# Kernel tuning notes

Hardware: AMD Instinct MI355X
Metric: run time of the kernel (lower is better)

Reference implementation:

```python
import math
import jax, jax.numpy as jnp
import numpy as np

NUM_HEADS = 16
LN_EPS = 1e-5


def _ln(x, g, b):
    m = x.mean(-1, keepdims=True)
    v = ((x - m) ** 2).mean(-1, keepdims=True)
    return (x - m) * jax.lax.rsqrt(v + LN_EPS) * g + b


def _rotary_embedding(lat, lon, dim, base=10000.0):
    # spherical-geometry-aware rotary phases; returns sin/cos of shape lat.shape + [dim//2]
    pi = jnp.asarray(math.pi, lat.dtype)
    lon_wrapped = jnp.remainder(lon + pi, 2 * pi) - pi
    lat_c = jnp.clip(lat, -math.pi / 2 + 1e-6, math.pi / 2 - 1e-6)
    scaled_lon = lon_wrapped * jnp.cos(lat_c)
    half = dim // 2
    inv_freq = 1.0 / (base ** (jnp.arange(half, dtype=lat.dtype) / half))
    phase = (lat_c + scaled_lon)[..., None] * inv_freq
    return jnp.sin(phase), jnp.cos(phase)


def _apply_rotary(q, k, sin, cos):
    # q,k: [N, heads, S, hd]; sin/cos: [S, hd//2]
    sin = sin[None, None]
    cos = cos[None, None]
    def rot(x):
        x1 = x[..., 0::2]  # even lanes (torch view(...,hd//2,2).unbind(-1))
        x2 = x[..., 1::2]
        # torch concatenates the two rotated halves (no re-interleave)
        return jnp.concatenate([x1 * cos - x2 * sin, x1 * sin + x2 * cos], axis=-1)
    return rot(q), rot(k)


def _sdpa(q, k, v):
    scale = 1.0 / jnp.sqrt(jnp.asarray(q.shape[-1], q.dtype))
    s = jnp.einsum('nhqd,nhkd->nhqk', q, k) * scale
    return jnp.einsum('nhqk,nhkd->nhqd', jax.nn.softmax(s, axis=-1), v)


def _axial_block(tokens, g, bln, qkv_w, qkv_b, proj_w, proj_b, sincos):
    # tokens: [N, S, D] -> norm -> qkv -> (rope) -> sdpa -> proj -> residual
    N, S, D = tokens.shape
    hd = D // NUM_HEADS
    qkv = _ln(tokens, g, bln) @ qkv_w + qkv_b
    q, k, v = jnp.split(qkv, 3, axis=-1)
    def to_heads(t):
        return t.reshape(N, S, NUM_HEADS, hd).transpose(0, 2, 1, 3)
    q, k, v = to_heads(q), to_heads(k), to_heads(v)
    if sincos is not None:
        q, k = _apply_rotary(q, k, sincos[0], sincos[1])
    o = _sdpa(q, k, v).transpose(0, 2, 1, 3).reshape(N, S, D)
    return tokens + (o @ proj_w + proj_b)


def setup_inputs() -> dict:
    key = jax.random.key(0)
    ks = jax.random.split(key, 8)
    B, L, H, W, D = 1, 13, 48, 96, 512
    x = jax.random.normal(ks[0], (B, L, H, W, D), dtype=jnp.float32)
    lat_grid = jnp.linspace(-math.pi / 2 + 0.01, math.pi / 2 - 0.01, H, dtype=jnp.float32)
    lon_grid = jnp.linspace(-math.pi, math.pi, W, dtype=jnp.float32)  # unused by forward
    s = 0.02
    return {
        'x': x, 'lat_grid': lat_grid, 'lon_grid': lon_grid,
        'lat_qkv_w': s * jax.random.normal(ks[1], (D, 3 * D), jnp.float32),
        'lat_qkv_b': jnp.zeros((3 * D,), jnp.float32),
        'lon_qkv_w': s * jax.random.normal(ks[2], (D, 3 * D), jnp.float32),
        'lon_qkv_b': jnp.zeros((3 * D,), jnp.float32),
        'lev_qkv_w': s * jax.random.normal(ks[3], (D, 3 * D), jnp.float32),
        'lev_qkv_b': jnp.zeros((3 * D,), jnp.float32),
        'proj_w': s * jax.random.normal(ks[4], (D, D), jnp.float32),
        'proj_b': jnp.zeros((D,), jnp.float32),
        'g_lat': jnp.ones((D,), jnp.float32), 'b_lat': jnp.zeros((D,), jnp.float32),
        'g_lon': jnp.ones((D,), jnp.float32), 'b_lon': jnp.zeros((D,), jnp.float32),
        'g_lev': jnp.ones((D,), jnp.float32), 'b_lev': jnp.zeros((D,), jnp.float32),
    }


def reference(x, lat_grid, lon_grid, lat_qkv_w, lat_qkv_b, lon_qkv_w, lon_qkv_b,
              lev_qkv_w, lev_qkv_b, proj_w, proj_b,
              g_lat, b_lat, g_lon, b_lon, g_lev, b_lev):
    B, L, H, W, D = x.shape
    hd = D // NUM_HEADS
    # --- lat axis ---
    lat_tokens = x.transpose(0, 1, 3, 2, 4).reshape(B * L * W, H, D)
    lat_sin, lat_cos = _rotary_embedding(lat_grid, jnp.zeros_like(lat_grid), hd)
    lat_out = _axial_block(lat_tokens, g_lat, b_lat, lat_qkv_w, lat_qkv_b,
                           proj_w, proj_b, (lat_sin, lat_cos))
    lat_out = lat_out.reshape(B, L, W, H, D).transpose(0, 1, 3, 2, 4)
    # --- lon axis ---
    lon_tokens = lat_out.reshape(B * L * H, W, D)
    lon_range = jnp.linspace(-math.pi, math.pi, W, dtype=x.dtype)
    lon_sin, lon_cos = _rotary_embedding(jnp.zeros_like(lon_range), lon_range, hd)
    lon_out = _axial_block(lon_tokens, g_lon, b_lon, lon_qkv_w, lon_qkv_b,
                           proj_w, proj_b, (lon_sin, lon_cos))
    lon_out = lon_out.reshape(B, L, H, W, D)
    # --- level axis (no rotary) ---
    lev_tokens = lon_out.transpose(0, 2, 3, 1, 4).reshape(B * H * W, L, D)
    lev_out = _axial_block(lev_tokens, g_lev, b_lev, lev_qkv_w, lev_qkv_b,
                           proj_w, proj_b, None)
    return lev_out.reshape(B, H, W, L, D).transpose(0, 3, 1, 2, 4)
```

## Files before the change

### kernel.cpp

```cpp
#include <hip/hip_runtime.h>
#include <cstdint>


#define L_DIM 13
#define H_DIM 48
#define W_DIM 96
#define D_DIM 512
#define NH    16
#define MTOK  (L_DIM * H_DIM * W_DIM)
#define N3    (3 * D_DIM)
#define PI_F  3.14159265358979323846f

typedef __bf16 bf16x8 __attribute__((ext_vector_type(8)));
typedef float  f32x4  __attribute__((ext_vector_type(4)));

__device__ __forceinline__ float bf2f(unsigned short u) {
    return __builtin_bit_cast(float, ((unsigned)u) << 16);
}
__device__ __forceinline__ unsigned short f2bf(float f) {
    unsigned u = __builtin_bit_cast(unsigned, f);
    u += 0x7fffu + ((u >> 16) & 1u);
    return (unsigned short)(u >> 16);
}
__device__ __forceinline__ void gload16(unsigned short* lds, const unsigned short* g) {
    __builtin_amdgcn_global_load_lds(
        (const __attribute__((address_space(1))) unsigned int*)g,
        (__attribute__((address_space(3))) unsigned int*)lds, 16, 0, 0);
}

__global__ __launch_bounds__(256) void transpose_w(const float* __restrict__ w,
                                                   unsigned short* __restrict__ wt, int N) {
    __shared__ unsigned short t[64][65];
    const int k0 = blockIdx.x * 64, n0 = blockIdx.y * 64;
    const int tid = threadIdx.x;
    #pragma unroll
    for (int j = 0; j < 16; ++j) {
        int lin = j * 256 + tid;
        int kr = lin >> 6, nc = lin & 63;
        t[kr][nc] = f2bf(w[(size_t)(k0 + kr) * N + n0 + nc]);
    }
    __syncthreads();
    #pragma unroll
    for (int j = 0; j < 16; ++j) {
        int lin = j * 256 + tid;
        int nr = lin >> 6, kc = lin & 63;
        wt[(size_t)(n0 + nr) * 512 + k0 + kc] = t[kc][nr];
    }
}

__global__ __launch_bounds__(256) void ln_apply(
    const float* __restrict__ src, const float* __restrict__ g,
    const float* __restrict__ bln, unsigned short* __restrict__ out)
{
    int wv = threadIdx.x >> 6, lane = threadIdx.x & 63;
    int t = blockIdx.x * 4 + wv;
    const float* p = src + (size_t)t * 512 + lane * 8;
    float4 a = *(const float4*)p, b = *(const float4*)(p + 4);
    float s  = a.x + a.y + a.z + a.w + b.x + b.y + b.z + b.w;
    float s2 = a.x*a.x + a.y*a.y + a.z*a.z + a.w*a.w + b.x*b.x + b.y*b.y + b.z*b.z + b.w*b.w;
    #pragma unroll
    for (int off = 1; off < 64; off <<= 1) {
        s  += __shfl_xor(s, off, 64);
        s2 += __shfl_xor(s2, off, 64);
    }
    float mu = s * (1.f / 512.f);
    float rs = rsqrtf(s2 * (1.f / 512.f) - mu * mu + 1e-5f);
    float4 g0 = *(const float4*)(g + lane * 8),  g1 = *(const float4*)(g + lane * 8 + 4);
    float4 b0 = *(const float4*)(bln + lane * 8), b1 = *(const float4*)(bln + lane * 8 + 4);
    unsigned short o[8];
    o[0] = f2bf((a.x - mu) * rs * g0.x + b0.x);
    o[1] = f2bf((a.y - mu) * rs * g0.y + b0.y);
    o[2] = f2bf((a.z - mu) * rs * g0.z + b0.z);
    o[3] = f2bf((a.w - mu) * rs * g0.w + b0.w);
    o[4] = f2bf((b.x - mu) * rs * g1.x + b1.x);
    o[5] = f2bf((b.y - mu) * rs * g1.y + b1.y);
    o[6] = f2bf((b.z - mu) * rs * g1.z + b1.z);
    o[7] = f2bf((b.w - mu) * rs * g1.w + b1.w);
    uint4 r;
    r.x = (unsigned)o[0] | ((unsigned)o[1] << 16);
    r.y = (unsigned)o[2] | ((unsigned)o[3] << 16);
    r.z = (unsigned)o[4] | ((unsigned)o[5] << 16);
    r.w = (unsigned)o[6] | ((unsigned)o[7] << 16);
    *(uint4*)&out[(size_t)t * 512 + lane * 8] = r;
}

__global__ __launch_bounds__(256) void qkv_gemm(
    const unsigned short* __restrict__ lnb,
    const unsigned short* __restrict__ wT, const float* __restrict__ bias,
    unsigned short* __restrict__ out)
{
    __shared__ alignas(16) unsigned short As[128][64];
    __shared__ alignas(16) unsigned short Bs[128][64];
    const int n0 = blockIdx.x * 128, m0 = blockIdx.y * 128;
    const int tid = threadIdx.x, lane = tid & 63, wv = tid >> 6;
    const int wm = (wv >> 1) * 64, wn = (wv & 1) * 64;
    const int srow = lane >> 3;
    const int scol = (((lane & 7) ^ srow) << 3);
    f32x4 acc[4][4] = {};

    for (int k0 = 0; k0 < 512; k0 += 64) {
        #pragma unroll
        for (int i = 0; i < 4; ++i) {
            int c = i * 4 + wv;
            int r = c * 8 + srow;
            gload16(&As[c * 8][0], &lnb[(size_t)(m0 + r) * 512 + k0 + scol]);
            gload16(&Bs[c * 8][0], &wT [(size_t)(n0 + r) * 512 + k0 + scol]);
        }
        __syncthreads();
        const int ko = (lane >> 4) * 8, lm = lane & 15, sw = lm & 7;
        #pragma unroll
        for (int kk = 0; kk < 64; kk += 32) {
            const int cA = ((((kk + ko) >> 3) ^ sw) << 3);
            bf16x8 af[4], bfr[4];
            #pragma unroll
            for (int mi = 0; mi < 4; ++mi) af[mi]  = *(const bf16x8*)&As[wm + mi * 16 + lm][cA];
            #pragma unroll
            for (int ni = 0; ni < 4; ++ni) bfr[ni] = *(const bf16x8*)&Bs[wn + ni * 16 + lm][cA];
            #pragma unroll
            for (int mi = 0; mi < 4; ++mi)
                #pragma unroll
                for (int ni = 0; ni < 4; ++ni)
                    acc[mi][ni] = __builtin_amdgcn_mfma_f32_16x16x32_bf16(af[mi], bfr[ni], acc[mi][ni], 0, 0, 0);
        }
        __syncthreads();
    }
    const int cr = (lane >> 4) * 4, ccol = lane & 15;
    #pragma unroll
    for (int ni = 0; ni < 4; ++ni) {
        int col = n0 + wn + ni * 16 + ccol;
        float bb = bias[col];
        #pragma unroll
        for (int mi = 0; mi < 4; ++mi)
            #pragma unroll
            for (int r = 0; r < 4; ++r) {
                int row = m0 + wm + mi * 16 + cr + r;
                out[(size_t)row * N3 + col] = f2bf(acc[mi][ni][r] + bb);
            }
    }
}

template<int S, int MODE>
__global__ __launch_bounds__(256) void attn_big(
    unsigned short* __restrict__ qkv,
    const float* __restrict__ lat_grid, const float* __restrict__ lon_grid)
{
    constexpr int NQ  = S / 16;
    constexpr int SKP = (S + 31) & ~31;
    constexpr int VST = SKP + 8;
    __shared__ alignas(16) unsigned short qs[S][40];
    __shared__ alignas(16) unsigned short ks[S][40];
    __shared__ alignas(16) unsigned short vT[32][VST];
    __shared__ alignas(16) unsigned short pb[4][16][VST];

    const int n = blockIdx.x, h = blockIdx.y;
    const int tid = threadIdx.x, lane = tid & 63, wv = tid >> 6;
    int base, step;
    if (MODE == 0) { int l = n / 96, w = n - l * 96; base = l * 4608 + w; step = 96; }
    else           { base = n * 96; step = 1; }

    const float SCALE = 0.17677669529663689f;
    for (int idx = tid; idx < S * 16; idx += 256) {
        int s = idx >> 4, i = idx & 15;
        size_t ro = (size_t)(base + s * step) * N3 + h * 32;
        unsigned qp = *(const unsigned*)(qkv + ro + 2 * i);
        unsigned kp = *(const unsigned*)(qkv + ro + 512 + 2 * i);
        unsigned vp = *(const unsigned*)(qkv + ro + 1024 + 2 * i);
        float coord;
        if (MODE == 0) {
            float la = lat_grid[s];
            coord = fminf(fmaxf(la, -PI_F / 2 + 1e-6f), PI_F / 2 - 1e-6f);
        } else {
            float xp = lon_grid[s] + PI_F;
            coord = xp - floorf(xp * (0.5f / PI_F)) * (2.f * PI_F) - PI_F;
        }
        float ph = coord * exp2f(-(float)i * 0.83048202372f);
        float sn = sinf(ph), cs = cosf(ph);
        float q1 = bf2f((unsigned short)qp), q2 = bf2f((unsigned short)(qp >> 16));
        float k1 = bf2f((unsigned short)kp), k2 = bf2f((unsigned short)(kp >> 16));
        qs[s][i]      = f2bf((q1 * cs - q2 * sn) * SCALE);
        qs[s][16 + i] = f2bf((q1 * sn + q2 * cs) * SCALE);
        ks[s][i]      = f2bf(k1 * cs - k2 * sn);
        ks[s][16 + i] = f2bf(k1 * sn + k2 * cs);
        vT[2 * i][s]     = (unsigned short)vp;
        vT[2 * i + 1][s] = (unsigned short)(vp >> 16);
    }
    if (SKP > S) {
        for (int idx = tid; idx < 32 * (SKP - S); idx += 256)
            vT[idx / (SKP - S)][S + idx % (SKP - S)] = 0;
    }
    __syncthreads();

    const int lm = lane & 15, ko = (lane >> 4) * 8, q4 = (lane >> 4) * 4;
    f32x4 zero = {0.f, 0.f, 0.f, 0.f};
    bf16x8 vf[SKP / 32][2];
    #pragma unroll
    for (int u2 = 0; u2 < SKP / 32; ++u2)
        #pragma unroll
        for (int nh2 = 0; nh2 < 2; ++nh2)
            vf[u2][nh2] = *(const bf16x8*)&vT[nh2 * 16 + lm][u2 * 32 + ko];
    if (SKP > S) {
        for (int idx = lane; idx < 16 * (SKP - S); idx += 64)
            pb[wv][idx / (SKP - S)][S + idx % (SKP - S)] = 0;
    }

    for (int t = wv; t < NQ; t += 4) {
        bf16x8 aq = *(const bf16x8*)&qs[t * 16 + lm][ko];
        f32x4 c[NQ];
        #pragma unroll
        for (int u = 0; u < NQ; ++u) {
            bf16x8 bk = *(const bf16x8*)&ks[u * 16 + lm][ko];
            c[u] = __builtin_amdgcn_mfma_f32_16x16x32_bf16(aq, bk, zero, 0, 0, 0);
        }
        float mr[4] = {-1e30f, -1e30f, -1e30f, -1e30f}, sm[4] = {0.f, 0.f, 0.f, 0.f};
        #pragma unroll
        for (int u = 0; u < NQ; ++u)
            #pragma unroll
            for (int r = 0; r < 4; ++r) mr[r] = fmaxf(mr[r], c[u][r]);
        #pragma unroll
        for (int r = 0; r < 4; ++r)
            #pragma unroll
            for (int off = 1; off < 16; off <<= 1)
                mr[r] = fmaxf(mr[r], __shfl_xor(mr[r], off, 64));
        #pragma unroll
        for (int u = 0; u < NQ; ++u)
            #pragma unroll
            for (int r = 0; r < 4; ++r) {
                float e = __expf(c[u][r] - mr[r]);
                c[u][r] = e; sm[r] += e;
            }
        #pragma unroll
        for (int r = 0; r < 4; ++r) {
            #pragma unroll
            for (int off = 1; off < 16; off <<= 1)
                sm[r] += __shfl_xor(sm[r], off, 64);
            sm[r] = 1.f / sm[r];
        }
        #pragma unroll
        for (int u = 0; u < NQ; ++u)
            #pragma unroll
            for (int r = 0; r < 4; ++r)
                pb[wv][q4 + r][u * 16 + lm] = f2bf(c[u][r] * sm[r]);
        __builtin_amdgcn_wave_barrier();
        f32x4 o0 = zero, o1 = zero;
        #pragma unroll
        for (int u2 = 0; u2 < SKP / 32; ++u2) {
            bf16x8 ap = *(const bf16x8*)&pb[wv][lm][u2 * 32 + ko];
            o0 = __builtin_amdgcn_mfma_f32_16x16x32_bf16(ap, vf[u2][0], o0, 0, 0, 0);
            o1 = __builtin_amdgcn_mfma_f32_16x16x32_bf16(ap, vf[u2][1], o1, 0, 0, 0);
        }
        __builtin_amdgcn_wave_barrier();
        #pragma unroll
        for (int r = 0; r < 4; ++r) {
            int row = t * 16 + q4 + r;
            size_t ro = (size_t)(base + row * step) * N3 + h * 32;
            qkv[ro + lm]      = f2bf(o0[r]);
            qkv[ro + 16 + lm] = f2bf(o1[r]);
        }
    }
}

__global__ __launch_bounds__(256) void attn_small(unsigned short* __restrict__ qkv)
{
    __shared__ alignas(16) unsigned short qs[4][16][40];
    __shared__ alignas(16) unsigned short ks[4][16][40];
    __shared__ alignas(16) unsigned short vT[4][32][40];
    __shared__ alignas(16) unsigned short pb[4][16][40];
    const int tid = threadIdx.x, lane = tid & 63, wv = tid >> 6;
    const int pair = blockIdx.x * 4 + wv;
    const int n = pair >> 4, h = pair & 15;
    const int base = n, step = 4608;

    for (int idx = lane; idx < 13 * 16; idx += 64) {
        int s = idx >> 4, i = idx & 15;
        size_t ro = (size_t)(base + s * step) * N3 + h * 32;
        *(unsigned*)&qs[wv][s][2 * i] = *(const unsigned*)(qkv + ro + 2 * i);
        *(unsigned*)&ks[wv][s][2 * i] = *(const unsigned*)(qkv + ro + 512 + 2 * i);
        unsigned vp = *(const unsigned*)(qkv + ro + 1024 + 2 * i);
        vT[wv][2 * i][s]     = (unsigned short)vp;
        vT[wv][2 * i + 1][s] = (unsigned short)(vp >> 16);
    }
    for (int idx = lane; idx < 32 * 19; idx += 64) {
        int d = idx / 19, k = 13 + idx % 19;
        vT[wv][d][k] = 0;
    }
    for (int idx = lane; idx < 16 * 16; idx += 64)
        pb[wv][idx >> 4][16 + (idx & 15)] = 0;
    __syncthreads();

    const int lm = lane & 15, ko = (lane >> 4) * 8, q4 = (lane >> 4) * 4;
    f32x4 zero = {0.f, 0.f, 0.f, 0.f};
    bf16x8 aq = *(const bf16x8*)&qs[wv][lm][ko];
    bf16x8 bk = *(const bf16x8*)&ks[wv][lm][ko];
    f32x4 c = __builtin_amdgcn_mfma_f32_16x16x32_bf16(aq, bk, zero, 0, 0, 0);
    const float SCALE = 0.17677669529663689f;
    float cf[4], mr[4], sm[4];
    bool colok = (lm < 13);
    #pragma unroll
    for (int r = 0; r < 4; ++r) {
        cf[r] = colok ? c[r] * SCALE : -1e30f;
        mr[r] = cf[r];
    }
    #pragma unroll
    for (int r = 0; r < 4; ++r)
        #pragma unroll
        for (int off = 1; off < 16; off <<= 1)
            mr[r] = fmaxf(mr[r], __shfl_xor(mr[r], off, 64));
    #pragma unroll
    for (int r = 0; r < 4; ++r) { cf[r] = __expf(cf[r] - mr[r]); sm[r] = cf[r]; }
    #pragma unroll
    for (int r = 0; r < 4; ++r) {
        #pragma unroll
        for (int off = 1; off < 16; off <<= 1)
            sm[r] += __shfl_xor(sm[r], off, 64);
        sm[r] = 1.f / sm[r];
    }
    #pragma unroll
    for (int r = 0; r < 4; ++r)
        pb[wv][q4 + r][lm] = f2bf(cf[r] * sm[r]);
    __builtin_amdgcn_wave_barrier();
    bf16x8 ap  = *(const bf16x8*)&pb[wv][lm][ko];
    bf16x8 vf0 = *(const bf16x8*)&vT[wv][lm][ko];
    bf16x8 vf1 = *(const bf16x8*)&vT[wv][16 + lm][ko];
    f32x4 o0 = __builtin_amdgcn_mfma_f32_16x16x32_bf16(ap, vf0, zero, 0, 0, 0);
    f32x4 o1 = __builtin_amdgcn_mfma_f32_16x16x32_bf16(ap, vf1, zero, 0, 0, 0);
    #pragma unroll
    for (int r = 0; r < 4; ++r) {
        int row = q4 + r;
        if (row < 13) {
            size_t ro = (size_t)(base + row * step) * N3 + h * 32;
            qkv[ro + lm]      = f2bf(o0[r]);
            qkv[ro + 16 + lm] = f2bf(o1[r]);
        }
    }
}

__global__ __launch_bounds__(256) void proj_gemm(
    const unsigned short* __restrict__ attn,
    const unsigned short* __restrict__ pT, const float* __restrict__ pb,
    const float* __restrict__ resid, float* __restrict__ tok)
{
    __shared__ alignas(16) unsigned short As[128][64];
    __shared__ alignas(16) unsigned short Bs[128][64];
    const int n0 = blockIdx.x * 128, m0 = blockIdx.y * 128;
    const int tid = threadIdx.x, lane = tid & 63, wv = tid >> 6;
    const int wm = (wv >> 1) * 64, wn = (wv & 1) * 64;
    const int srow = lane >> 3;
    const int scol = (((lane & 7) ^ srow) << 3);
    f32x4 acc[4][4] = {};

    for (int k0 = 0; k0 < 512; k0 += 64) {
        #pragma unroll
        for (int i = 0; i < 4; ++i) {
            int c = i * 4 + wv;
            int r = c * 8 + srow;
            gload16(&As[c * 8][0], &attn[(size_t)(m0 + r) * N3 + k0 + scol]);
            gload16(&Bs[c * 8][0], &pT [(size_t)(n0 + r) * 512 + k0 + scol]);
        }
        __syncthreads();
        const int ko = (lane >> 4) * 8, lm = lane & 15, sw = lm & 7;
        #pragma unroll
        for (int kk = 0; kk < 64; kk += 32) {
            const int cA = ((((kk + ko) >> 3) ^ sw) << 3);
            bf16x8 af[4], bfr[4];
            #pragma unroll
            for (int mi = 0; mi < 4; ++mi) af[mi]  = *(const bf16x8*)&As[wm + mi * 16 + lm][cA];
            #pragma unroll
            for (int ni = 0; ni < 4; ++ni) bfr[ni] = *(const bf16x8*)&Bs[wn + ni * 16 + lm][cA];
            #pragma unroll
            for (int mi = 0; mi < 4; ++mi)
                #pragma unroll
                for (int ni = 0; ni < 4; ++ni)
                    acc[mi][ni] = __builtin_amdgcn_mfma_f32_16x16x32_bf16(af[mi], bfr[ni], acc[mi][ni], 0, 0, 0);
        }
        __syncthreads();
    }
    const int cr = (lane >> 4) * 4, ccol = lane & 15;
    #pragma unroll
    for (int ni = 0; ni < 4; ++ni) {
        int col = n0 + wn + ni * 16 + ccol;
        float bb = pb[col];
        #pragma unroll
        for (int mi = 0; mi < 4; ++mi)
            #pragma unroll
            for (int r = 0; r < 4; ++r) {
                int row = m0 + wm + mi * 16 + cr + r;
                size_t a = (size_t)row * 512 + col;
                tok[a] = resid[a] + acc[mi][ni][r] + bb;
            }
    }
}

extern "C" void kernel_launch(void* const* d_in, const int* in_sizes, int n_in,
                              void* d_out, int out_size, void* d_ws, size_t ws_size,
                              hipStream_t stream) {
    const float* x        = (const float*)d_in[0];
    const float* lat_grid = (const float*)d_in[1];
    const float* lon_grid = (const float*)d_in[2];
    const float* qkv_w[3] = {(const float*)d_in[3], (const float*)d_in[5], (const float*)d_in[7]};
    const float* qkv_b[3] = {(const float*)d_in[4], (const float*)d_in[6], (const float*)d_in[8]};
    const float* proj_w   = (const float*)d_in[9];
    const float* proj_b   = (const float*)d_in[10];
    const float* g[3]     = {(const float*)d_in[11], (const float*)d_in[13], (const float*)d_in[15]};
    const float* bln[3]   = {(const float*)d_in[12], (const float*)d_in[14], (const float*)d_in[16]};
    float* tok = (float*)d_out;

    unsigned short* wT0 = (unsigned short*)d_ws;
    unsigned short* wT1 = wT0 + 1536 * 512;
    unsigned short* wT2 = wT1 + 1536 * 512;
    unsigned short* pT  = wT2 + 1536 * 512;
    unsigned short* lnb = pT + 512 * 512;
    unsigned short* qkv = lnb + (size_t)MTOK * 512;
    unsigned short* wT[3] = {wT0, wT1, wT2};

    transpose_w<<<dim3(8, 24), 256, 0, stream>>>(qkv_w[0], wT0, 1536);
    transpose_w<<<dim3(8, 24), 256, 0, stream>>>(qkv_w[1], wT1, 1536);
    transpose_w<<<dim3(8, 24), 256, 0, stream>>>(qkv_w[2], wT2, 1536);
    transpose_w<<<dim3(8, 8),  256, 0, stream>>>(proj_w, pT, 512);

    for (int b = 0; b < 3; ++b) {
        const float* src = (b == 0) ? x : tok;
        ln_apply<<<MTOK / 4, 256, 0, stream>>>(src, g[b], bln[b], lnb);
        qkv_gemm<<<dim3(N3 / 128, MTOK / 128), 256, 0, stream>>>(lnb, wT[b], qkv_b[b], qkv);
        if (b == 0)
            attn_big<48, 0><<<dim3(L_DIM * W_DIM, NH), 256, 0, stream>>>(qkv, lat_grid, lon_grid);
        else if (b == 1)
            attn_big<96, 1><<<dim3(L_DIM * H_DIM, NH), 256, 0, stream>>>(qkv, lat_grid, lon_grid);
        else
            attn_small<<<(H_DIM * W_DIM * NH) / 4, 256, 0, stream>>>(qkv);
        proj_gemm<<<dim3(512 / 128, MTOK / 128), 256, 0, stream>>>(qkv, pT, proj_b, src, tok);
    }
}
```

Before: 1.239 ms.

## Replace QKV and projection GEMMs with double-buffered 256x256 pipelined MFMA kernel

Both GEMMs are replaced by one templated kernel that uses 256x256 tiles, 8 waves, and double-buffered LDS, so global loads for the next K tile overlap MFMA work on the current one. It adds XCD-aware block swizzling, s_setprio around MFMA bursts, and vectorized epilogue stores (packed bf16 and float4 residual add). The aim is to cut the memory-stall and barrier overhead of the single-buffered 128x128 kernels. The trade-off is more LDS per block, fewer blocks in flight, and delicate manual vmcnt/barrier sequencing.

```diff
diff --git a/kernel.cpp b/kernel.cpp
--- a/kernel.cpp
+++ b/kernel.cpp
@@ -84,58 +84,146 @@
     *(uint4*)&out[(size_t)t * 512 + lane * 8] = r;
 }
 
-__global__ __launch_bounds__(256) void qkv_gemm(
-    const unsigned short* __restrict__ lnb,
-    const unsigned short* __restrict__ wT, const float* __restrict__ bias,
-    unsigned short* __restrict__ out)
+#define QUAD(mi, A) do { \
+    acc[mi][0] = __builtin_amdgcn_mfma_f32_16x16x32_bf16(b0, A, acc[mi][0], 0, 0, 0); \
+    acc[mi][1] = __builtin_amdgcn_mfma_f32_16x16x32_bf16(b1, A, acc[mi][1], 0, 0, 0); \
+    acc[mi][2] = __builtin_amdgcn_mfma_f32_16x16x32_bf16(b2, A, acc[mi][2], 0, 0, 0); \
+    acc[mi][3] = __builtin_amdgcn_mfma_f32_16x16x32_bf16(b3, A, acc[mi][3], 0, 0, 0); \
+} while (0)
+#define RDA(mi, ks) (*(const bf16x8*)&As[cur][wm + (mi) * 16 + lm][((((ks) * 4 + kq) ^ (lm & 7)) << 3)])
+#define RDB(ni, ks) (*(const bf16x8*)&Bs[cur][wn + (ni) * 16 + lm][((((ks) * 4 + kq) ^ (lm & 7)) << 3)])
+
+template<int LDA, int NBX, bool PROJ>
+__global__ __launch_bounds__(512, 2) void gemm8p(
+    const unsigned short* __restrict__ A,
+    const unsigned short* __restrict__ B,
+    const float* __restrict__ bias,
+    const float* __restrict__ resid,
+    float* __restrict__ outf,
+    unsigned short* __restrict__ outh)
 {
-    __shared__ alignas(16) unsigned short As[128][64];
-    __shared__ alignas(16) unsigned short Bs[128][64];
-    const int n0 = blockIdx.x * 128, m0 = blockIdx.y * 128;
+    __shared__ alignas(16) unsigned short As[2][256][64];
+    __shared__ alignas(16) unsigned short Bs[2][256][64];
+
+    const int nwg = NBX * 234;
+    const int orig = blockIdx.y * NBX + blockIdx.x;
+    const int qq = nwg >> 3, rr = nwg & 7;
+    const int xcd = orig & 7, idx = orig >> 3;
+    const int swz = (xcd < rr ? xcd * (qq + 1) : rr * (qq + 1) + (xcd - rr) * qq) + idx;
+    const int n0 = (swz % NBX) * 256;
+    const int m0 = (swz / NBX) * 256;
+
     const int tid = threadIdx.x, lane = tid & 63, wv = tid >> 6;
-    const int wm = (wv >> 1) * 64, wn = (wv & 1) * 64;
-    const int srow = lane >> 3;
-    const int scol = (((lane & 7) ^ srow) << 3);
-    f32x4 acc[4][4] = {};
-
-    for (int k0 = 0; k0 < 512; k0 += 64) {
-        #pragma unroll
-        for (int i = 0; i < 4; ++i) {
-            int c = i * 4 + wv;
-            int r = c * 8 + srow;
-            gload16(&As[c * 8][0], &lnb[(size_t)(m0 + r) * 512 + k0 + scol]);
-            gload16(&Bs[c * 8][0], &wT [(size_t)(n0 + r) * 512 + k0 + scol]);
-        }
-        __syncthreads();
-        const int ko = (lane >> 4) * 8, lm = lane & 15, sw = lm & 7;
-        #pragma unroll
-        for (int kk = 0; kk < 64; kk += 32) {
-            const int cA = ((((kk + ko) >> 3) ^ sw) << 3);
-            bf16x8 af[4], bfr[4];
-            #pragma unroll
-            for (int mi = 0; mi < 4; ++mi) af[mi]  = *(const bf16x8*)&As[wm + mi * 16 + lm][cA];
-            #pragma unroll
-            for (int ni = 0; ni < 4; ++ni) bfr[ni] = *(const bf16x8*)&Bs[wn + ni * 16 + lm][cA];
-            #pragma unroll
-            for (int mi = 0; mi < 4; ++mi)
-                #pragma unroll
-                for (int ni = 0; ni < 4; ++ni)
-                    acc[mi][ni] = __builtin_amdgcn_mfma_f32_16x16x32_bf16(af[mi], bfr[ni], acc[mi][ni], 0, 0, 0);
-        }
-        __syncthreads();
-    }
-    const int cr = (lane >> 4) * 4, ccol = lane & 15;
-    #pragma unroll
-    for (int ni = 0; ni < 4; ++ni) {
-        int col = n0 + wn + ni * 16 + ccol;
-        float bb = bias[col];
-        #pragma unroll
-        for (int mi = 0; mi < 4; ++mi)
-            #pragma unroll
-            for (int r = 0; r < 4; ++r) {
-                int row = m0 + wm + mi * 16 + cr + r;
-                out[(size_t)row * N3 + col] = f2bf(acc[mi][ni][r] + bb);
+    const int wm = (wv >> 2) * 128, wn = (wv & 3) * 64;
+    const int lm = lane & 15, kq = lane >> 4;
+    const int rblk = lane >> 3;
+    const int sc = (((lane & 7) ^ rblk) << 3);
+
+    const unsigned short* bsrc = B + (size_t)(n0 + wv * 32 + rblk) * 512 + sc;
+    const int ar0 = (wv & 4) ? (128 + (wv & 3) * 16) : (wv * 16);
+    const unsigned short* asrc = A + (size_t)(m0 + ar0 + rblk) * LDA + sc;
+
+    f32x4 acc[8][4] = {};
+
+    #pragma unroll
+    for (int j = 0; j < 4; ++j)
+        gload16(&Bs[0][wv * 32 + j * 8][0], bsrc + (size_t)(j * 8) * 512);
+    gload16(&As[0][ar0 + 0][0], asrc);
+    gload16(&As[0][ar0 + 8][0], asrc + (size_t)8 * LDA);
+    gload16(&As[0][ar0 + 64][0], asrc + (size_t)64 * LDA);
+    gload16(&As[0][ar0 + 72][0], asrc + (size_t)72 * LDA);
+    asm volatile("s_waitcnt vmcnt(2)" ::: "memory");
+    __builtin_amdgcn_s_barrier();
+    __builtin_amdgcn_sched_barrier(0);
+
+    for (int kt = 0; kt < 8; ++kt) {
+        const int cur = kt & 1, nxt = cur ^ 1;
+        const int kn = (kt + 1) * 64;
+        const bool st = (kt < 7);
+        bf16x8 a0, a1, a2, a3, b0, b1, b2, b3;
+
+        a0 = RDA(0, 0); a1 = RDA(1, 0); a2 = RDA(2, 0); a3 = RDA(3, 0);
+        b0 = RDB(0, 0); b1 = RDB(1, 0); b2 = RDB(2, 0); b3 = RDB(3, 0);
+        if (st) {
+            gload16(&Bs[nxt][wv * 32 +  0][0], bsrc + (size_t) 0 * 512 + kn);
+            gload16(&Bs[nxt][wv * 32 +  8][0], bsrc + (size_t) 8 * 512 + kn);
+            gload16(&Bs[nxt][wv * 32 + 16][0], bsrc + (size_t)16 * 512 + kn);
+            gload16(&Bs[nxt][wv * 32 + 24][0], bsrc + (size_t)24 * 512 + kn);
+        }
+        __builtin_amdgcn_s_barrier();
+        __builtin_amdgcn_s_setprio(1);
+        QUAD(0, a0); QUAD(1, a1); QUAD(2, a2); QUAD(3, a3);
+        __builtin_amdgcn_s_setprio(0);
+        if (st) asm volatile("s_waitcnt vmcnt(4)" ::: "memory");
+        else    asm volatile("s_waitcnt vmcnt(0)" ::: "memory");
+        __builtin_amdgcn_s_barrier();
+        __builtin_amdgcn_sched_barrier(0);
+
+        a0 = RDA(4, 0); a1 = RDA(5, 0); a2 = RDA(6, 0); a3 = RDA(7, 0);
+        if (st) {
+            gload16(&As[nxt][ar0 + 0][0], asrc + kn);
+            gload16(&As[nxt][ar0 + 8][0], asrc + (size_t)8 * LDA + kn);
+        }
+        __builtin_amdgcn_s_barrier();
+        __builtin_amdgcn_s_setprio(1);
+        QUAD(4, a0); QUAD(5, a1); QUAD(6, a2); QUAD(7, a3);
+        __builtin_amdgcn_s_setprio(0);
+        __builtin_amdgcn_s_barrier();
+
+        a0 = RDA(0, 1); a1 = RDA(1, 1); a2 = RDA(2, 1); a3 = RDA(3, 1);
+        b0 = RDB(0, 1); b1 = RDB(1, 1); b2 = RDB(2, 1); b3 = RDB(3, 1);
+        if (st) {
+            gload16(&As[nxt][ar0 + 64][0], asrc + (size_t)64 * LDA + kn);
+            gload16(&As[nxt][ar0 + 72][0], asrc + (size_t)72 * LDA + kn);
+        }
+        __builtin_amdgcn_s_barrier();
+        __builtin_amdgcn_s_setprio(1);
+        QUAD(0, a0); QUAD(1, a1); QUAD(2, a2); QUAD(3, a3);
+        __builtin_amdgcn_s_setprio(0);
+        __builtin_amdgcn_s_barrier();
+
+        a0 = RDA(4, 1); a1 = RDA(5, 1); a2 = RDA(6, 1); a3 = RDA(7, 1);
+        __builtin_amdgcn_s_barrier();
+        __builtin_amdgcn_s_setprio(1);
+        QUAD(4, a0); QUAD(5, a1); QUAD(6, a2); QUAD(7, a3);
+        __builtin_amdgcn_s_setprio(0);
+        asm volatile("s_waitcnt vmcnt(2)" ::: "memory");
+        __builtin_amdgcn_s_barrier();
+        __builtin_amdgcn_sched_barrier(0);
+    }
+
+    const int cr = kq << 2;
+    if constexpr (!PROJ) {
+        #pragma unroll
+        for (int ni = 0; ni < 4; ++ni) {
+            const int col = n0 + wn + ni * 16 + cr;
+            const float4 bb = *(const float4*)&bias[col];
+            #pragma unroll
+            for (int mi = 0; mi < 8; ++mi) {
+                const size_t off = (size_t)(m0 + wm + mi * 16 + lm) * N3 + col;
+                uint2 pk;
+                pk.x = (unsigned)f2bf(acc[mi][ni][0] + bb.x) | ((unsigned)f2bf(acc[mi][ni][1] + bb.y) << 16);
+                pk.y = (unsigned)f2bf(acc[mi][ni][2] + bb.z) | ((unsigned)f2bf(acc[mi][ni][3] + bb.w) << 16);
+                *(uint2*)&outh[off] = pk;
             }
+        }
+    } else {
+        #pragma unroll
+        for (int ni = 0; ni < 4; ++ni) {
+            const int col = n0 + wn + ni * 16 + cr;
+            const float4 bb = *(const float4*)&bias[col];
+            #pragma unroll
+            for (int mi = 0; mi < 8; ++mi) {
+                const size_t off = (size_t)(m0 + wm + mi * 16 + lm) * 512 + col;
+                float4 rs = *(const float4*)&resid[off];
+                float4 o;
+                o.x = rs.x + acc[mi][ni][0] + bb.x;
+                o.y = rs.y + acc[mi][ni][1] + bb.y;
+                o.z = rs.z + acc[mi][ni][2] + bb.z;
+                o.w = rs.w + acc[mi][ni][3] + bb.w;
+                *(float4*)&outf[off] = o;
+            }
+        }
     }
 }
 
@@ -334,62 +422,6 @@
     }
 }
 
-__global__ __launch_bounds__(256) void proj_gemm(
-    const unsigned short* __restrict__ attn,
-    const unsigned short* __restrict__ pT, const float* __restrict__ pb,
-    const float* __restrict__ resid, float* __restrict__ tok)
-{
-    __shared__ alignas(16) unsigned short As[128][64];
-    __shared__ alignas(16) unsigned short Bs[128][64];
-    const int n0 = blockIdx.x * 128, m0 = blockIdx.y * 128;
-    const int tid = threadIdx.x, lane = tid & 63, wv = tid >> 6;
-    const int wm = (wv >> 1) * 64, wn = (wv & 1) * 64;
-    const int srow = lane >> 3;
-    const int scol = (((lane & 7) ^ srow) << 3);
-    f32x4 acc[4][4] = {};
-
-    for (int k0 = 0; k0 < 512; k0 += 64) {
-        #pragma unroll
-        for (int i = 0; i < 4; ++i) {
-            int c = i * 4 + wv;
-            int r = c * 8 + srow;
-            gload16(&As[c * 8][0], &attn[(size_t)(m0 + r) * N3 + k0 + scol]);
-            gload16(&Bs[c * 8][0], &pT [(size_t)(n0 + r) * 512 + k0 + scol]);
-        }
-        __syncthreads();
-        const int ko = (lane >> 4) * 8, lm = lane & 15, sw = lm & 7;
-        #pragma unroll
-        for (int kk = 0; kk < 64; kk += 32) {
-            const int cA = ((((kk + ko) >> 3) ^ sw) << 3);
-            bf16x8 af[4], bfr[4];
-            #pragma unroll
-            for (int mi = 0; mi < 4; ++mi) af[mi]  = *(const bf16x8*)&As[wm + mi * 16 + lm][cA];
-            #pragma unroll
-            for (int ni = 0; ni < 4; ++ni) bfr[ni] = *(const bf16x8*)&Bs[wn + ni * 16 + lm][cA];
-            #pragma unroll
-            for (int mi = 0; mi < 4; ++mi)
-                #pragma unroll
-                for (int ni = 0; ni < 4; ++ni)
-                    acc[mi][ni] = __builtin_amdgcn_mfma_f32_16x16x32_bf16(af[mi], bfr[ni], acc[mi][ni], 0, 0, 0);
-        }
-        __syncthreads();
-    }
-    const int cr = (lane >> 4) * 4, ccol = lane & 15;
-    #pragma unroll
-    for (int ni = 0; ni < 4; ++ni) {
-        int col = n0 + wn + ni * 16 + ccol;
-        float bb = pb[col];
-        #pragma unroll
-        for (int mi = 0; mi < 4; ++mi)
-            #pragma unroll
-            for (int r = 0; r < 4; ++r) {
-                int row = m0 + wm + mi * 16 + cr + r;
-                size_t a = (size_t)row * 512 + col;
-                tok[a] = resid[a] + acc[mi][ni][r] + bb;
-            }
-    }
-}
-
 extern "C" void kernel_launch(void* const* d_in, const int* in_sizes, int n_in,
                               void* d_out, int out_size, void* d_ws, size_t ws_size,
                               hipStream_t stream) {
@@ -420,13 +452,15 @@
     for (int b = 0; b < 3; ++b) {
         const float* src = (b == 0) ? x : tok;
         ln_apply<<<MTOK / 4, 256, 0, stream>>>(src, g[b], bln[b], lnb);
-        qkv_gemm<<<dim3(N3 / 128, MTOK / 128), 256, 0, stream>>>(lnb, wT[b], qkv_b[b], qkv);
+        gemm8p<512, 6, false><<<dim3(6, MTOK / 256), 512, 0, stream>>>(
+            lnb, wT[b], qkv_b[b], nullptr, nullptr, qkv);
         if (b == 0)
             attn_big<48, 0><<<dim3(L_DIM * W_DIM, NH), 256, 0, stream>>>(qkv, lat_grid, lon_grid);
         else if (b == 1)
             attn_big<96, 1><<<dim3(L_DIM * H_DIM, NH), 256, 0, stream>>>(qkv, lat_grid, lon_grid);
         else
             attn_small<<<(H_DIM * W_DIM * NH) / 4, 256, 0, stream>>>(qkv);
-        proj_gemm<<<dim3(512 / 128, MTOK / 128), 256, 0, stream>>>(qkv, pT, proj_b, src, tok);
-    }
-}
+        gemm8p<1536, 2, true><<<dim3(2, MTOK / 256), 512, 0, stream>>>(
+            qkv, pT, proj_b, src, tok, nullptr);
+    }
+}
```

Measured after the change: 1.267 ms. 1.02x slower.
